# Performance work log

Hardware: AMD Instinct MI355X
Metric: run time of the kernel (lower is better)

The kernel has to match this reference:

```python
import jax, jax.numpy as jnp
import numpy as np

N_NODES = 100000
N_EDGES = 1600000
IN_C, HID_C, OUT_C = 512, 128, 40


def gcn_conv(x, edge_index):
    """Symmetric-normalized sparse aggregation: out[d] = sum_e 1/sqrt(deg[s]*deg[d]) * x[s]."""
    n = x.shape[0]
    src, dst = edge_index[0], edge_index[1]
    deg = jax.ops.segment_sum(jnp.ones_like(dst, dtype=x.dtype), dst, num_segments=n)
    deg = jnp.maximum(deg, 1.0)  # guard isolated nodes
    dinv = jax.lax.rsqrt(deg)
    w = dinv[src] * dinv[dst]                      # [E]
    msg = x[src] * w[:, None]                      # [E, C] gather + scale
    return jax.ops.segment_sum(msg, dst, num_segments=n)  # scatter-add -> [N, C]


def setup_inputs() -> dict:
    key = jax.random.key(0)
    k1, k2, k3, k4 = jax.random.split(key, 4)
    x = jax.random.normal(k1, (N_NODES, IN_C), dtype=jnp.float32)
    edge_index = jax.random.randint(k2, (2, N_EDGES), 0, N_NODES, dtype=jnp.int64)
    # xavier_uniform with gain=1.414 (as in reset_parameters), zero biases
    def xavier(k, shape, gain=1.414):
        fan_out, fan_in = shape
        bound = gain * np.sqrt(6.0 / (fan_in + fan_out))
        return jax.random.uniform(k, shape, jnp.float32, -bound, bound)
    W0 = xavier(k3, (HID_C, IN_C))
    b0 = jnp.zeros((HID_C,), jnp.float32)
    W1 = xavier(k4, (OUT_C, HID_C))
    b1 = jnp.zeros((OUT_C,), jnp.float32)
    return {"x": x, "edge_index": edge_index, "W0": W0, "b0": b0, "W1": W1, "b1": b1}


def reference(x, edge_index, W0, b0, W1, b1):
    # layer 0: project -> sparse aggregate -> bias -> relu (dropout off in eval)
    h = x @ W0.T
    h = gcn_conv(h, edge_index)
    h = jax.nn.relu(h + b0)
    # final layer: project -> sparse aggregate -> bias (no activation)
    h = h @ W1.T
    h = gcn_conv(h, edge_index)
    return h + b1
```

## Files before the change

kernel.cpp:

```cpp
#include <hip/hip_runtime.h>
#include <hip/hip_bf16.h>
#include <cstddef>

#define N_NODES 100000
#define N_EDGES 1600000
#define IN_C 512
#define HID_C 128
#define OUT_C 40
#define OUT_CP 48
#define EPB 8000
#define NPART 200
#define NBKT 196
#define BSHIFT 9

typedef short bf16x8 __attribute__((ext_vector_type(8)));
typedef float f32x4 __attribute__((ext_vector_type(4)));

__device__ __forceinline__ float bf2f(unsigned short u) {
    union { unsigned int i; float f; } v; v.i = ((unsigned int)u) << 16; return v.f;
}
__device__ __forceinline__ float bf2f_lo(unsigned int u) {
    union { unsigned int i; float f; } v; v.i = u << 16; return v.f;
}
__device__ __forceinline__ float bf2f_hi(unsigned int u) {
    union { unsigned int i; float f; } v; v.i = u & 0xFFFF0000u; return v.f;
}
__device__ __forceinline__ unsigned short f2bf(float f) {
    union { float f; unsigned int i; } v; v.f = f;
    unsigned int x = v.i;
    return (unsigned short)((x + 0x7FFFu + ((x >> 16) & 1u)) >> 16);
}

__device__ __forceinline__ void glds16(const void* g, void* l) {
    __builtin_amdgcn_global_load_lds(
        (const __attribute__((address_space(1))) unsigned int*)g,
        (__attribute__((address_space(3))) unsigned int*)l,
        16, 0, 0);
}

__global__ void k_detect(const unsigned int* __restrict__ xbits,
                         const int* __restrict__ ei32, int* __restrict__ flags) {
    if (threadIdx.x == 0 && blockIdx.x == 0) {
        int inrange = 0;
        for (int i = 0; i < 64; i++) {
            unsigned int b = xbits[i * 33 + 1];
            int e = (int)((b >> 23) & 0xFFu);
            if (e >= 90 && e <= 160) inrange++;
        }
        flags[0] = (inrange >= 32) ? 0 : 1;
        int zeros = 0;
        for (int i = 0; i < 8; i++) if (ei32[2 * i + 1] == 0) zeros++;
        flags[1] = (zeros == 8) ? 1 : 0;
    }
}

__device__ __forceinline__ int load_src(const int* ei, int mi, int e) {
    return mi ? ei[2 * e] : ei[e];
}
__device__ __forceinline__ int load_dst(const int* ei, int mi, int e) {
    return mi ? ei[2 * (N_EDGES + e)] : ei[N_EDGES + e];
}

#define NW_TOTAL (IN_C * HID_C + HID_C * OUT_C + HID_C + OUT_C)
__global__ void k_norm_w(const void* __restrict__ W0, const void* __restrict__ W1,
                         const void* __restrict__ b0, const void* __restrict__ b1,
                         const int* __restrict__ flags,
                         unsigned short* __restrict__ w0n, unsigned short* __restrict__ w1n,
                         float* __restrict__ b0n, float* __restrict__ b1n) {
    int mf = flags[0];
    int i = blockIdx.x * 256 + threadIdx.x;
    if (i >= NW_TOTAL) return;
    if (i < IN_C * HID_C) {
        w0n[i] = mf ? ((const unsigned short*)W0)[i] : f2bf(((const float*)W0)[i]);
    } else if (i < IN_C * HID_C + HID_C * OUT_C) {
        int j = i - IN_C * HID_C;
        w1n[j] = mf ? ((const unsigned short*)W1)[j] : f2bf(((const float*)W1)[j]);
    } else if (i < IN_C * HID_C + HID_C * OUT_C + HID_C) {
        int j = i - IN_C * HID_C - HID_C * OUT_C;
        b0n[j] = mf ? bf2f(((const unsigned short*)b0)[j]) : ((const float*)b0)[j];
    } else {
        int j = i - IN_C * HID_C - HID_C * OUT_C - HID_C;
        b1n[j] = mf ? bf2f(((const unsigned short*)b1)[j]) : ((const float*)b1)[j];
    }
}

__global__ __launch_bounds__(256) void k_part1(const int* __restrict__ ei,
                                               const int* __restrict__ flags,
                                               int* __restrict__ bcnt,
                                               int* __restrict__ block_off) {
    __shared__ int h[NBKT];
    int t = threadIdx.x;
    for (int i = t; i < NBKT; i += 256) h[i] = 0;
    __syncthreads();
    int mi = flags[1];
    int base = blockIdx.x * EPB;
    for (int j = t; j < EPB; j += 256) {
        int e = base + j;
        if (e < N_EDGES) atomicAdd(&h[load_dst(ei, mi, e) >> BSHIFT], 1);
    }
    __syncthreads();
    for (int i = t; i < NBKT; i += 256)
        block_off[blockIdx.x * NBKT + i] = atomicAdd(&bcnt[i], h[i]);
}

__global__ void k_scan_bkt(const int* __restrict__ bcnt, int* __restrict__ bbase) {
    __shared__ int sm[256];
    int t = threadIdx.x;
    int v = (t < NBKT) ? bcnt[t] : 0;
    sm[t] = v; __syncthreads();
    for (int off = 1; off < 256; off <<= 1) {
        int a = (t >= off) ? sm[t - off] : 0;
        __syncthreads();
        sm[t] += a;
        __syncthreads();
    }
    if (t < NBKT) bbase[t] = sm[t] - v;
    if (t == NBKT - 1) bbase[NBKT] = sm[t];
}

__global__ __launch_bounds__(256) void k_part2(const int* __restrict__ ei,
                                               const int* __restrict__ flags,
                                               const int* __restrict__ bbase,
                                               const int* __restrict__ block_off,
                                               unsigned int* __restrict__ bedges) {
    __shared__ int cur[NBKT];
    int t = threadIdx.x;
    for (int i = t; i < NBKT; i += 256)
        cur[i] = bbase[i] + block_off[blockIdx.x * NBKT + i];
    __syncthreads();
    int mi = flags[1];
    int base = blockIdx.x * EPB;
    for (int j = t; j < EPB; j += 256) {
        int e = base + j;
        if (e < N_EDGES) {
            int d = load_dst(ei, mi, e);
            int s = load_src(ei, mi, e);
            int p = atomicAdd(&cur[d >> BSHIFT], 1);
            bedges[p] = ((unsigned int)s << BSHIFT) | (unsigned int)(d & 511);
        }
    }
}

__global__ __launch_bounds__(512) void k_bucket_csr(const unsigned int* __restrict__ bedges,
                                                    const int* __restrict__ bbase,
                                                    int* __restrict__ rowptr,
                                                    float* __restrict__ dinv,
                                                    int* __restrict__ col) {
    __shared__ int cnt[512];
    __shared__ int cur[512];
    int b = blockIdx.x, t = threadIdx.x;
    int ebeg = bbase[b], eend = bbase[b + 1];
    cnt[t] = 0;
    __syncthreads();
    for (int j = ebeg + t; j < eend; j += 512)
        atomicAdd(&cnt[bedges[j] & 511], 1);
    __syncthreads();
    int v = cnt[t];
    cur[t] = v; __syncthreads();
    for (int off = 1; off < 512; off <<= 1) {
        int a = (t >= off) ? cur[t - off] : 0;
        __syncthreads();
        cur[t] += a;
        __syncthreads();
    }
    int excl = cur[t] - v;
    int node = b * 512 + t;
    if (node < N_NODES) {
        rowptr[node] = ebeg + excl;
        float dd = (float)v; if (dd < 1.f) dd = 1.f;
        dinv[node] = rsqrtf(dd);
    } else if (node == N_NODES) {
        rowptr[N_NODES] = ebeg + excl;
    }
    __syncthreads();
    cur[t] = ebeg + excl;
    __syncthreads();
    for (int j = ebeg + t; j < eend; j += 512) {
        unsigned int pk = bedges[j];
        int p = atomicAdd(&cur[pk & 511], 1);
        col[p] = (int)(pk >> BSHIFT);
    }
}

#define G1_BUF 24576
#define G1_BOFF 16384

__device__ __forceinline__ void gemm1_f32_async(const float* __restrict__ xg,
                                                const unsigned short* __restrict__ w0n,
                                                unsigned short* __restrict__ h1,
                                                char* __restrict__ smem,
                                                int node0, int t) {
    const int w = t >> 6;
    const int lane = t & 63;
    const int r16 = lane & 15;
    const int quad = lane >> 4;

    f32x4 acc[2][8];
#pragma unroll
    for (int m = 0; m < 2; m++)
#pragma unroll
        for (int c = 0; c < 8; c++) acc[m][c] = (f32x4){0.f, 0.f, 0.f, 0.f};

    const int lrow = lane >> 3;
    const int lch = (lane & 7) ^ lrow;
    const float* pa[4];
#pragma unroll
    for (int g = 0; g < 4; g++) {
        int r = node0 + w * 32 + 8 * g + lrow;
        if (r >= N_NODES) r = N_NODES - 1;
        pa[g] = xg + (size_t)r * IN_C + lch * 4;
    }
    const unsigned short* pb[2];
#pragma unroll
    for (int g = 0; g < 2; g++)
        pb[g] = w0n + (size_t)((2 * w + g) * 16 + r16) * IN_C + quad * 8;

    auto stage = [&](int buf, int ks) {
        char* Ab = smem + buf * G1_BUF + w * 4096;
        char* Bb = smem + buf * G1_BUF + G1_BOFF + w * 2048;
        glds16(pa[0] + ks, Ab);
        glds16(pa[1] + ks, Ab + 1024);
        glds16(pa[2] + ks, Ab + 2048);
        glds16(pa[3] + ks, Ab + 3072);
        glds16(pb[0] + ks, Bb);
        glds16(pb[1] + ks, Bb + 1024);
    };

    const int swz = r16 & 7;

    auto compute = [&](int buf) {
        const char* Ab = smem + buf * G1_BUF;
        const char* Bb = Ab + G1_BOFF;
        bf16x8 a[2];
#pragma unroll
        for (int m = 0; m < 2; m++) {
            int rowb = (w * 32 + m * 16 + r16) * 128;
            int c0 = ((2 * quad) ^ swz) * 16;
            int c1 = ((2 * quad + 1) ^ swz) * 16;
            float4 fa = *reinterpret_cast<const float4*>(Ab + rowb + c0);
            float4 fb = *reinterpret_cast<const float4*>(Ab + rowb + c1);
            a[m] = (bf16x8){(short)f2bf(fa.x), (short)f2bf(fa.y), (short)f2bf(fa.z), (short)f2bf(fa.w),
                            (short)f2bf(fb.x), (short)f2bf(fb.y), (short)f2bf(fb.z), (short)f2bf(fb.w)};
        }
#pragma unroll
        for (int ct = 0; ct < 8; ct++) {
            bf16x8 b = *reinterpret_cast<const bf16x8*>(Bb + ct * 1024 + lane * 16);
            acc[0][ct] = __builtin_amdgcn_mfma_f32_16x16x32_bf16(a[0], b, acc[0][ct], 0, 0, 0);
            acc[1][ct] = __builtin_amdgcn_mfma_f32_16x16x32_bf16(a[1], b, acc[1][ct], 0, 0, 0);
        }
    };

    stage(0, 0);
    __syncthreads();
    for (int tt = 0; tt < 15; ++tt) {
        int cur = tt & 1;
        stage(cur ^ 1, (tt + 1) * 32);
        compute(cur);
        __syncthreads();
    }
    compute(1);

#pragma unroll
    for (int m = 0; m < 2; m++) {
#pragma unroll
        for (int ct = 0; ct < 8; ct++) {
#pragma unroll
            for (int r = 0; r < 4; r++) {
                int row = node0 + w * 32 + m * 16 + quad * 4 + r;
                if (row < N_NODES)
                    h1[(size_t)row * HID_C + ct * 16 + r16] = f2bf(acc[m][ct][r]);
            }
        }
    }
}

__device__ __forceinline__ void gemm1_bf16_async(const unsigned short* __restrict__ xg,
                                                 const unsigned short* __restrict__ w0n,
                                                 unsigned short* __restrict__ h1,
                                                 unsigned short* __restrict__ smem,
                                                 int node0, int t) {
    const int w = t >> 6;
    const int lane = t & 63;
    const int r16 = lane & 15;
    const int quad = lane >> 4;

    f32x4 acc[2][8];
#pragma unroll
    for (int m = 0; m < 2; m++)
#pragma unroll
        for (int c = 0; c < 8; c++) acc[m][c] = (f32x4){0.f, 0.f, 0.f, 0.f};

    int rA0 = node0 + (2 * w) * 16 + r16;     if (rA0 >= N_NODES) rA0 = N_NODES - 1;
    int rA1 = node0 + (2 * w + 1) * 16 + r16; if (rA1 >= N_NODES) rA1 = N_NODES - 1;
    const unsigned short* pa0 = xg + (size_t)rA0 * IN_C + quad * 8;
    const unsigned short* pa1 = xg + (size_t)rA1 * IN_C + quad * 8;
    const unsigned short* pb0 = w0n + (size_t)((2 * w) * 16 + r16) * IN_C + quad * 8;
    const unsigned short* pb1 = w0n + (size_t)((2 * w + 1) * 16 + r16) * IN_C + quad * 8;

    auto stage = [&](int buf, int ks) {
        unsigned short* a = smem + buf * 8192 + (2 * w) * 512;
        glds16(pa0 + ks, a);
        glds16(pa1 + ks, a + 512);
        glds16(pb0 + ks, a + 4096);
        glds16(pb1 + ks, a + 4096 + 512);
    };

    const int fo = quad * 128 + r16 * 8;

    auto compute = [&](int buf) {
        const unsigned short* Ab = smem + buf * 8192;
        const unsigned short* Bb = Ab + 4096;
        bf16x8 a0 = *reinterpret_cast<const bf16x8*>(Ab + (2 * w) * 512 + fo);
        bf16x8 a1 = *reinterpret_cast<const bf16x8*>(Ab + (2 * w + 1) * 512 + fo);
#pragma unroll
        for (int ct = 0; ct < 8; ct++) {
            bf16x8 b = *reinterpret_cast<const bf16x8*>(Bb + ct * 512 + fo);
            acc[0][ct] = __builtin_amdgcn_mfma_f32_16x16x32_bf16(a0, b, acc[0][ct], 0, 0, 0);
            acc[1][ct] = __builtin_amdgcn_mfma_f32_16x16x32_bf16(a1, b, acc[1][ct], 0, 0, 0);
        }
    };

    stage(0, 0);
    __syncthreads();
    for (int tt = 0; tt < 15; ++tt) {
        int cur = tt & 1;
        stage(cur ^ 1, (tt + 1) * 32);
        compute(cur);
        __syncthreads();
    }
    compute(1);

#pragma unroll
    for (int m = 0; m < 2; m++) {
#pragma unroll
        for (int ct = 0; ct < 8; ct++) {
#pragma unroll
            for (int r = 0; r < 4; r++) {
                int row = node0 + w * 32 + m * 16 + quad * 4 + r;
                if (row < N_NODES)
                    h1[(size_t)row * HID_C + ct * 16 + r16] = f2bf(acc[m][ct][r]);
            }
        }
    }
}

__global__ __launch_bounds__(256, 3) void k_gemm1(const void* __restrict__ x,
                                                  const unsigned short* __restrict__ w0n,
                                                  const int* __restrict__ flags,
                                                  unsigned short* __restrict__ h1) {
    __shared__ __align__(16) char smem[2 * G1_BUF];
    int node0 = blockIdx.x * 128;
    int t = threadIdx.x;
    if (flags[0]) gemm1_bf16_async((const unsigned short*)x, w0n, h1,
                                   (unsigned short*)smem, node0, t);
    else          gemm1_f32_async((const float*)x, w0n, h1, smem, node0, t);
}

__global__ __launch_bounds__(256) void k_agg1(const int* __restrict__ rowptr,
                                              const int* __restrict__ col,
                                              const float* __restrict__ dinv,
                                              const unsigned int* __restrict__ h1v,
                                              const float* __restrict__ b0n,
                                              unsigned int* __restrict__ h2v) {
    int w = threadIdx.x >> 6;
    int lane = threadIdx.x & 63;
    int d = blockIdx.x * 4 + w;
    if (d >= N_NODES) return;
    int beg = rowptr[d], end = rowptr[d + 1];
    float a0 = 0.f, a1 = 0.f;
    int j = beg;
    for (; j + 8 <= end; j += 8) {
        int s[8];
        float wj[8];
        unsigned int r[8];
#pragma unroll
        for (int q = 0; q < 8; q++) s[q] = col[j + q];
#pragma unroll
        for (int q = 0; q < 8; q++) wj[q] = dinv[s[q]];
#pragma unroll
        for (int q = 0; q < 8; q++) r[q] = h1v[(size_t)s[q] * 64 + lane];
#pragma unroll
        for (int q = 0; q < 8; q++) {
            a0 += wj[q] * bf2f_lo(r[q]);
            a1 += wj[q] * bf2f_hi(r[q]);
        }
    }
    for (; j < end; j++) {
        int s = col[j];
        float wj = dinv[s];
        unsigned int r = h1v[(size_t)s * 64 + lane];
        a0 += wj * bf2f_lo(r);
        a1 += wj * bf2f_hi(r);
    }
    float dv = dinv[d];
    float o0 = a0 * dv + b0n[2 * lane];
    float o1 = a1 * dv + b0n[2 * lane + 1];
    o0 = o0 > 0.f ? o0 : 0.f;
    o1 = o1 > 0.f ? o1 : 0.f;
    h2v[(size_t)d * 64 + lane] = (unsigned int)f2bf(o0) | ((unsigned int)f2bf(o1) << 16);
}

__global__ __launch_bounds__(256) void k_gemm2(const unsigned short* __restrict__ h2,
                                               const unsigned short* __restrict__ w1p,
                                               float* __restrict__ p2) {
    int wave = (blockIdx.x * 256 + (int)threadIdx.x) >> 6;
    if (wave >= N_NODES / 16) return;
    int lane = threadIdx.x & 63;
    int r16 = lane & 15;
    int quad = lane >> 4;
    int node_base = wave * 16;

    f32x4 acc[3];
#pragma unroll
    for (int c = 0; c < 3; c++) acc[c] = (f32x4){0.f, 0.f, 0.f, 0.f};

    const unsigned short* arow = h2 + (size_t)(node_base + r16) * HID_C + quad * 8;
    const unsigned short* brow = w1p + (size_t)r16 * HID_C + quad * 8;

#pragma unroll
    for (int k0 = 0; k0 < HID_C; k0 += 32) {
        bf16x8 a = *reinterpret_cast<const bf16x8*>(arow + k0);
#pragma unroll
        for (int ct = 0; ct < 3; ct++) {
            bf16x8 b = *reinterpret_cast<const bf16x8*>(brow + (size_t)ct * 16 * HID_C + k0);
            acc[ct] = __builtin_amdgcn_mfma_f32_16x16x32_bf16(a, b, acc[ct], 0, 0, 0);
        }
    }

#pragma unroll
    for (int ct = 0; ct < 3; ct++) {
        int chan = ct * 16 + r16;
        if (chan < OUT_C) {
#pragma unroll
            for (int r = 0; r < 4; r++) {
                p2[(size_t)(node_base + quad * 4 + r) * OUT_C + chan] = acc[ct][r];
            }
        }
    }
}

__global__ __launch_bounds__(256) void k_agg2(const int* __restrict__ rowptr,
                                              const int* __restrict__ col,
                                              const float* __restrict__ dinv,
                                              const float* __restrict__ p2,
                                              const float* __restrict__ b1n,
                                              const int* __restrict__ flags,
                                              void* __restrict__ out) {
    int w = threadIdx.x >> 6;
    int lane = threadIdx.x & 63;
    int d = blockIdx.x * 4 + w;
    if (d >= N_NODES || lane >= OUT_C) return;
    int beg = rowptr[d], end = rowptr[d + 1];
    float acc = 0.f;
    int j = beg;
    for (; j + 8 <= end; j += 8) {
        int s[8];
        float wj[8], r[8];
#pragma unroll
        for (int q = 0; q < 8; q++) s[q] = col[j + q];
#pragma unroll
        for (int q = 0; q < 8; q++) wj[q] = dinv[s[q]];
#pragma unroll
        for (int q = 0; q < 8; q++) r[q] = p2[(size_t)s[q] * OUT_C + lane];
#pragma unroll
        for (int q = 0; q < 8; q++) acc += wj[q] * r[q];
    }
    for (; j < end; j++) {
        int s = col[j];
        acc += dinv[s] * p2[(size_t)s * OUT_C + lane];
    }
    float v = acc * dinv[d] + b1n[lane];
    size_t idx = (size_t)d * OUT_C + lane;
    if (flags[0]) ((unsigned short*)out)[idx] = f2bf(v);
    else          ((float*)out)[idx] = v;
}

extern "C" void kernel_launch(void* const* d_in, const int* in_sizes, int n_in,
                              void* d_out, int out_size, void* d_ws, size_t ws_size,
                              hipStream_t stream) {
    const void* x  = d_in[0];
    const int* ei  = (const int*)d_in[1];
    const void* W0 = d_in[2];
    const void* b0 = d_in[3];
    const void* W1 = d_in[4];
    const void* b1 = d_in[5];

    char* ws = (char*)d_ws;
    size_t off = 0;
    auto alloc = [&](size_t bytes) {
        char* p = ws + off;
        off += (bytes + 511) & ~(size_t)511;
        return p;
    };
    int*   flags   = (int*)  alloc(sizeof(int) * 2);
    int*   rowptr  = (int*)  alloc(sizeof(int) * (N_NODES + 1));
    float* dinv    = (float*)alloc(sizeof(float) * N_NODES);
    int*   col     = (int*)  alloc(sizeof(int) * N_EDGES);
    int*   bcnt    = (int*)  alloc(sizeof(int) * NBKT);
    int*   bbase   = (int*)  alloc(sizeof(int) * (NBKT + 1));
    int*   bloff   = (int*)  alloc(sizeof(int) * NPART * NBKT);
    unsigned int* bedges = (unsigned int*)alloc(sizeof(unsigned int) * N_EDGES);
    unsigned short* w0n = (unsigned short*)alloc(sizeof(unsigned short) * IN_C * HID_C);
    unsigned short* w1n = (unsigned short*)alloc(sizeof(unsigned short) * OUT_CP * HID_C);
    float* b0n = (float*)alloc(sizeof(float) * HID_C);
    float* b1n = (float*)alloc(sizeof(float) * OUT_C);
    unsigned short* h1 = (unsigned short*)alloc(sizeof(unsigned short) * (size_t)N_NODES * HID_C);
    unsigned short* h2 = (unsigned short*)alloc(sizeof(unsigned short) * (size_t)N_NODES * HID_C);
    float* p2 = (float*)h1;

    k_detect<<<1, 64, 0, stream>>>((const unsigned int*)x, ei, flags);
    hipMemsetAsync(w1n, 0, sizeof(unsigned short) * OUT_CP * HID_C, stream);
    k_norm_w<<<(NW_TOTAL + 255) / 256, 256, 0, stream>>>(W0, W1, b0, b1, flags, w0n, w1n, b0n, b1n);

    hipMemsetAsync(bcnt, 0, sizeof(int) * NBKT, stream);
    k_part1<<<NPART, 256, 0, stream>>>(ei, flags, bcnt, bloff);
    k_scan_bkt<<<1, 256, 0, stream>>>(bcnt, bbase);
    k_part2<<<NPART, 256, 0, stream>>>(ei, flags, bbase, bloff, bedges);
    k_bucket_csr<<<NBKT, 512, 0, stream>>>(bedges, bbase, rowptr, dinv, col);

    k_gemm1<<<(N_NODES + 127) / 128, 256, 0, stream>>>(x, w0n, flags, h1);
    k_agg1<<<(N_NODES + 3) / 4, 256, 0, stream>>>(rowptr, col, dinv,
                                                  (const unsigned int*)h1, b0n,
                                                  (unsigned int*)h2);
    k_gemm2<<<(N_NODES / 16 + 3) / 4, 256, 0, stream>>>(h2, w1n, p2);
    k_agg2<<<(N_NODES + 3) / 4, 256, 0, stream>>>(rowptr, col, dinv, p2, b1n, flags, d_out);
}
```

Measured before the change: 543.6 us.

## Fold source-degree normalization into GEMM epilogues and deepen gemm1 async pipeline

Pre-scales each projected row by dinv[src] in the gemm1 and gemm2 epilogues, so the aggregation kernels no longer gather dinv[s] per edge and only do plain sums. Separately, the fp32 gemm1 path is restructured to keep two stages of global loads in flight, using explicit vmcnt waits and raw s_barrier instead of __syncthreads. This removes a dependent random gather per edge in both aggregations. The cost is extra rounding, since the bf16 h1 now stores scaled values, plus hand-tuned waitcnt logic that must match the number of loads per stage.

Result: no change. 533.9 us (-1.8%).

```diff
diff --git a/kernel.cpp b/kernel.cpp
--- a/kernel.cpp
+++ b/kernel.cpp
@@ -187,6 +187,7 @@
 
 __device__ __forceinline__ void gemm1_f32_async(const float* __restrict__ xg,
                                                 const unsigned short* __restrict__ w0n,
+                                                const float* __restrict__ dinv,
                                                 unsigned short* __restrict__ h1,
                                                 char* __restrict__ smem,
                                                 int node0, int t) {
@@ -251,24 +252,34 @@
     };
 
     stage(0, 0);
-    __syncthreads();
-    for (int tt = 0; tt < 15; ++tt) {
-        int cur = tt & 1;
-        stage(cur ^ 1, (tt + 1) * 32);
-        compute(cur);
-        __syncthreads();
-    }
+    stage(1, 32);
+    for (int tt = 0; tt < 14; ++tt) {
+        asm volatile("s_waitcnt vmcnt(6)" ::: "memory");
+        __builtin_amdgcn_sched_barrier(0);
+        __builtin_amdgcn_s_barrier();
+        compute(tt & 1);
+        __builtin_amdgcn_s_barrier();
+        stage(tt & 1, (tt + 2) * 32);
+    }
+    asm volatile("s_waitcnt vmcnt(6)" ::: "memory");
+    __builtin_amdgcn_sched_barrier(0);
+    __builtin_amdgcn_s_barrier();
+    compute(0);
+    asm volatile("s_waitcnt vmcnt(0)" ::: "memory");
+    __builtin_amdgcn_sched_barrier(0);
+    __builtin_amdgcn_s_barrier();
     compute(1);
 
 #pragma unroll
     for (int m = 0; m < 2; m++) {
 #pragma unroll
-        for (int ct = 0; ct < 8; ct++) {
-#pragma unroll
-            for (int r = 0; r < 4; r++) {
-                int row = node0 + w * 32 + m * 16 + quad * 4 + r;
-                if (row < N_NODES)
-                    h1[(size_t)row * HID_C + ct * 16 + r16] = f2bf(acc[m][ct][r]);
+        for (int r = 0; r < 4; r++) {
+            int row = node0 + w * 32 + m * 16 + quad * 4 + r;
+            if (row < N_NODES) {
+                float dv = dinv[row];
+#pragma unroll
+                for (int ct = 0; ct < 8; ct++)
+                    h1[(size_t)row * HID_C + ct * 16 + r16] = f2bf(acc[m][ct][r] * dv);
             }
         }
     }
@@ -276,6 +287,7 @@
 
 __device__ __forceinline__ void gemm1_bf16_async(const unsigned short* __restrict__ xg,
                                                  const unsigned short* __restrict__ w0n,
+                                                 const float* __restrict__ dinv,
                                                  unsigned short* __restrict__ h1,
                                                  unsigned short* __restrict__ smem,
                                                  int node0, int t) {
@@ -333,12 +345,13 @@
 #pragma unroll
     for (int m = 0; m < 2; m++) {
 #pragma unroll
-        for (int ct = 0; ct < 8; ct++) {
-#pragma unroll
-            for (int r = 0; r < 4; r++) {
-                int row = node0 + w * 32 + m * 16 + quad * 4 + r;
-                if (row < N_NODES)
-                    h1[(size_t)row * HID_C + ct * 16 + r16] = f2bf(acc[m][ct][r]);
+        for (int r = 0; r < 4; r++) {
+            int row = node0 + w * 32 + m * 16 + quad * 4 + r;
+            if (row < N_NODES) {
+                float dv = dinv[row];
+#pragma unroll
+                for (int ct = 0; ct < 8; ct++)
+                    h1[(size_t)row * HID_C + ct * 16 + r16] = f2bf(acc[m][ct][r] * dv);
             }
         }
     }
@@ -347,13 +360,14 @@
 __global__ __launch_bounds__(256, 3) void k_gemm1(const void* __restrict__ x,
                                                   const unsigned short* __restrict__ w0n,
                                                   const int* __restrict__ flags,
+                                                  const float* __restrict__ dinv,
                                                   unsigned short* __restrict__ h1) {
     __shared__ __align__(16) char smem[2 * G1_BUF];
     int node0 = blockIdx.x * 128;
     int t = threadIdx.x;
-    if (flags[0]) gemm1_bf16_async((const unsigned short*)x, w0n, h1,
+    if (flags[0]) gemm1_bf16_async((const unsigned short*)x, w0n, dinv, h1,
                                    (unsigned short*)smem, node0, t);
-    else          gemm1_f32_async((const float*)x, w0n, h1, smem, node0, t);
+    else          gemm1_f32_async((const float*)x, w0n, dinv, h1, smem, node0, t);
 }
 
 __global__ __launch_bounds__(256) void k_agg1(const int* __restrict__ rowptr,
@@ -371,26 +385,21 @@
     int j = beg;
     for (; j + 8 <= end; j += 8) {
         int s[8];
-        float wj[8];
         unsigned int r[8];
 #pragma unroll
         for (int q = 0; q < 8; q++) s[q] = col[j + q];
 #pragma unroll
-        for (int q = 0; q < 8; q++) wj[q] = dinv[s[q]];
-#pragma unroll
         for (int q = 0; q < 8; q++) r[q] = h1v[(size_t)s[q] * 64 + lane];
 #pragma unroll
         for (int q = 0; q < 8; q++) {
-            a0 += wj[q] * bf2f_lo(r[q]);
-            a1 += wj[q] * bf2f_hi(r[q]);
+            a0 += bf2f_lo(r[q]);
+            a1 += bf2f_hi(r[q]);
         }
     }
     for (; j < end; j++) {
-        int s = col[j];
-        float wj = dinv[s];
-        unsigned int r = h1v[(size_t)s * 64 + lane];
-        a0 += wj * bf2f_lo(r);
-        a1 += wj * bf2f_hi(r);
+        unsigned int r = h1v[(size_t)col[j] * 64 + lane];
+        a0 += bf2f_lo(r);
+        a1 += bf2f_hi(r);
     }
     float dv = dinv[d];
     float o0 = a0 * dv + b0n[2 * lane];
@@ -402,6 +411,7 @@
 
 __global__ __launch_bounds__(256) void k_gemm2(const unsigned short* __restrict__ h2,
                                                const unsigned short* __restrict__ w1p,
+                                               const float* __restrict__ dinv,
                                                float* __restrict__ p2) {
     int wave = (blockIdx.x * 256 + (int)threadIdx.x) >> 6;
     if (wave >= N_NODES / 16) return;
@@ -427,13 +437,17 @@
         }
     }
 
+    float dv[4];
+#pragma unroll
+    for (int r = 0; r < 4; r++) dv[r] = dinv[node_base + quad * 4 + r];
+
 #pragma unroll
     for (int ct = 0; ct < 3; ct++) {
         int chan = ct * 16 + r16;
         if (chan < OUT_C) {
 #pragma unroll
             for (int r = 0; r < 4; r++) {
-                p2[(size_t)(node_base + quad * 4 + r) * OUT_C + chan] = acc[ct][r];
+                p2[(size_t)(node_base + quad * 4 + r) * OUT_C + chan] = acc[ct][r] * dv[r];
             }
         }
     }
@@ -455,19 +469,16 @@
     int j = beg;
     for (; j + 8 <= end; j += 8) {
         int s[8];
-        float wj[8], r[8];
+        float r[8];
 #pragma unroll
         for (int q = 0; q < 8; q++) s[q] = col[j + q];
 #pragma unroll
-        for (int q = 0; q < 8; q++) wj[q] = dinv[s[q]];
-#pragma unroll
         for (int q = 0; q < 8; q++) r[q] = p2[(size_t)s[q] * OUT_C + lane];
 #pragma unroll
-        for (int q = 0; q < 8; q++) acc += wj[q] * r[q];
+        for (int q = 0; q < 8; q++) acc += r[q];
     }
     for (; j < end; j++) {
-        int s = col[j];
-        acc += dinv[s] * p2[(size_t)s * OUT_C + lane];
+        acc += p2[(size_t)col[j] * OUT_C + lane];
     }
     float v = acc * dinv[d] + b1n[lane];
     size_t idx = (size_t)d * OUT_C + lane;
@@ -518,10 +529,10 @@
     k_part2<<<NPART, 256, 0, stream>>>(ei, flags, bbase, bloff, bedges);
     k_bucket_csr<<<NBKT, 512, 0, stream>>>(bedges, bbase, rowptr, dinv, col);
 
-    k_gemm1<<<(N_NODES + 127) / 128, 256, 0, stream>>>(x, w0n, flags, h1);
+    k_gemm1<<<(N_NODES + 127) / 128, 256, 0, stream>>>(x, w0n, flags, dinv, h1);
     k_agg1<<<(N_NODES + 3) / 4, 256, 0, stream>>>(rowptr, col, dinv,
                                                   (const unsigned int*)h1, b0n,
                                                   (unsigned int*)h2);
-    k_gemm2<<<(N_NODES / 16 + 3) / 4, 256, 0, stream>>>(h2, w1n, p2);
+    k_gemm2<<<(N_NODES / 16 + 3) / 4, 256, 0, stream>>>(h2, w1n, dinv, p2);
     k_agg2<<<(N_NODES + 3) / 4, 256, 0, stream>>>(rowptr, col, dinv, p2, b1n, flags, d_out);
 }
```
